# Kernel tuning notes

Measured on AMD Instinct MI355X. Metric: run time of the kernel, lower is better.

The kernel has to match this reference:

```python
import jax, jax.numpy as jnp
import numpy as np

EPS = 1e-12


def setup_inputs() -> dict:
    key = jax.random.key(0)
    k = jax.random.split(key, 6)
    B, C, T, A = 8, 1536, 4096, 128
    x = jax.random.normal(k[0], (B, C, T), dtype=jnp.float32)
    lengths = jax.random.randint(k[1], (B,), T // 2, T + 1, dtype=jnp.int64)
    W1 = jax.random.normal(k[2], (A, 3 * C), dtype=jnp.float32) * (1.0 / np.sqrt(3 * C))
    b1 = jax.random.normal(k[3], (A,), dtype=jnp.float32) * 0.01
    W2 = jax.random.normal(k[4], (1, A), dtype=jnp.float32) * (1.0 / np.sqrt(A))
    b2 = jax.random.normal(k[5], (1,), dtype=jnp.float32) * 0.01
    return {"x": x, "lengths": lengths, "W1": W1, "b1": b1, "W2": W2, "b2": b2}


def reference(x, lengths, W1, b1, W2, b2):
    # x: [B, C, T]
    B, C, T = x.shape
    mask = (jnp.arange(T)[None, :] < lengths[:, None]).astype(x.dtype)  # [B, T]
    m3 = mask[:, None, :]  # [B, 1, T]

    # causal (cumulative) mean / std for global context
    count = jnp.clip(jnp.cumsum(mask, axis=1), 1.0)[:, None, :]        # [B, 1, T]
    causal_mean = jnp.cumsum(x * m3, axis=2) / count                   # [B, C, T]
    causal_var = jnp.cumsum(x * x * m3, axis=2) / count - causal_mean ** 2
    causal_std = jnp.sqrt(jnp.clip(causal_var, EPS))

    attn_in = jnp.concatenate([x, causal_mean, causal_std], axis=1)    # [B, 3C, T]
    attn_in = attn_in.transpose(0, 2, 1)                               # [B, T, 3C]

    h = jnp.tanh(attn_in @ W1.T + b1)                                  # [B, T, A]
    logits = (h @ W2.T + b2)[..., 0]                                   # [B, T]

    # logits are query-independent, so causal softmax row q is
    # exp(l_k) / cumsum(exp(l))_q for k <= q -> O(T*C) prefix scan.
    e = jnp.exp(logits - jnp.max(logits, axis=1, keepdims=True))       # [B, T]
    Z = jnp.cumsum(e, axis=1)[:, None, :]                              # [B, 1, T]
    ew = e[:, None, :]                                                 # [B, 1, T]

    weighted_mean = jnp.cumsum(ew * x, axis=2) / Z                     # [B, C, T]
    sq_diff = (x - weighted_mean) ** 2
    weighted_var = jnp.cumsum(ew * sq_diff, axis=2) / Z
    weighted_std = jnp.sqrt(jnp.clip(weighted_var, EPS))

    # each causal softmax row sums to 1 -> final weights are 1/(T+eps)
    fw = 1.0 / (jnp.asarray(T, x.dtype) + EPS)
    final_mean = jnp.sum(weighted_mean, axis=2) * fw                   # [B, C]
    final_std = jnp.sum(weighted_std, axis=2) * fw
    return jnp.concatenate([final_mean, final_std], axis=1)            # [B, 2C]
```

## Files before the change

kernel.cpp:

```cpp
#include <hip/hip_runtime.h>
#include <hip/hip_bf16.h>

#define B_ 8
#define C_ 1536
#define T_ 4096
#define A_ 128
#define K3_ 4608
#define M32_ 128
#define KP_ 200

typedef _Float16 h8  __attribute__((ext_vector_type(8)));
typedef _Float16 h2v __attribute__((ext_vector_type(2)));
typedef float    f4  __attribute__((ext_vector_type(4)));

__global__ void k0_pack(const float* __restrict__ W1, _Float16* __restrict__ W1f) {
    int i = blockIdx.x * 256 + threadIdx.x;
    if (i >= A_ * K3_) return;
    int a = i / K3_, k = i - a * K3_;
    int t8 = a >> 4, r15 = a & 15;
    int kb = k >> 5, q = (k >> 3) & 3, j = k & 7;
    int lane = q * 16 + r15;
    W1f[(size_t)((kb * 8 + t8) * 64 + lane) * 8 + j] = (_Float16)W1[i];
}

__global__ __launch_bounds__(256) void k1_carry(
    const float* __restrict__ x, const int* __restrict__ lens,
    float2* __restrict__ carry)
{
    const int rowid = blockIdx.x * 4 + (threadIdx.x >> 6);
    const int lane  = threadIdx.x & 63;
    const int b     = rowid / C_;
    const int len   = lens[b];
    const float* xr = x + (size_t)rowid * T_;
    float2* cp = carry + (size_t)rowid * M32_;

    const int grp = lane >> 3;
    float base1 = 0.f, base2 = 0.f;

#pragma unroll
    for (int g = 0; g < 16; ++g) {
        const int t0g = g * 256;
        if (t0g >= len) {
            if ((lane & 7) == 0) cp[g * 8 + grp] = make_float2(base1, base2);
            continue;
        }
        float4 v = *(const float4*)(xr + t0g + lane * 4);
        float s1, s2;
        if (t0g + 256 <= len) {
            s1 = v.x + v.y + v.z + v.w;
            s2 = v.x * v.x + v.y * v.y + v.z * v.z + v.w * v.w;
        } else {
            const int tb = t0g + lane * 4;
            float vs[4] = {v.x, v.y, v.z, v.w};
            s1 = 0.f; s2 = 0.f;
#pragma unroll
            for (int j = 0; j < 4; ++j) {
                float m = (tb + j < len) ? vs[j] : 0.f;
                s1 += m; s2 += m * vs[j];
            }
        }
        float g1 = s1, g2 = s2;
        g1 += __shfl_xor(g1, 1, 64); g2 += __shfl_xor(g2, 1, 64);
        g1 += __shfl_xor(g1, 2, 64); g2 += __shfl_xor(g2, 2, 64);
        g1 += __shfl_xor(g1, 4, 64); g2 += __shfl_xor(g2, 4, 64);
        float V1 = g1, V2 = g2;
#pragma unroll
        for (int d = 8; d < 64; d <<= 1) {
            float o1 = __shfl_up(V1, d, 64);
            float o2 = __shfl_up(V2, d, 64);
            if (lane >= d) { V1 += o1; V2 += o2; }
        }
        const float e1 = V1 - g1, e2 = V2 - g2;
        if ((lane & 7) == 0) {
            cp[g * 8 + grp] = make_float2(base1 + e1, base2 + e2);
        }
        base1 += __shfl(V1, 63, 64);
        base2 += __shfl(V2, 63, 64);
    }
}

__global__ __launch_bounds__(256) void k2_gemm(
    const float* __restrict__ x, const int* __restrict__ lens,
    const float2* __restrict__ carry, const _Float16* __restrict__ W1f,
    const float* __restrict__ b1, const float* __restrict__ W2,
    float* __restrict__ logits)
{
    __shared__ _Float16 tile[32][KP_];
    __shared__ float s_w2[A_], s_b1[A_];
    __shared__ float lpart[2][32];

    const int tid = threadIdx.x;
    const int i    = blockIdx.x;
    const int mlow = i >> 7;
    const int b    = (i >> 4) & 7;
    const int m    = ((i & 15) << 3) | mlow;
    const int t0   = m << 5;
    const int len  = lens[b];

    if (tid < A_) { s_w2[tid] = W2[tid]; s_b1[tid] = b1[tid]; }

    const int cp  = tid >> 3;
    const int sgm = tid & 7;
    const int tb  = t0 + sgm * 4;

    const int lane = tid & 63;
    const int w    = tid >> 6;
    const int mtg  = w & 1;
    const int ntg  = w >> 1;
    const int ln15 = lane & 15, q = lane >> 4;
    const h8* W1f8 = (const h8*)W1f;

    f4 acc[4] = {};

    for (int c0 = 0; c0 < C_; c0 += 64) {
        const size_t rowA = (size_t)b * C_ + c0 + cp * 2;
        const float* xpA = x + rowA * T_ + tb;
        float4 va = *(const float4*)xpA;
        float4 vb = *(const float4*)(xpA + T_);
        float xa[4] = {va.x, va.y, va.z, va.w};
        float xb[4] = {vb.x, vb.y, vb.z, vb.w};
        float pA1[4], pA2[4], pB1[4], pB2[4];
        float a1 = 0.f, a2 = 0.f, c1 = 0.f, c2 = 0.f;
#pragma unroll
        for (int j = 0; j < 4; ++j) {
            bool in = (tb + j) < len;
            float ma = in ? xa[j] : 0.f;
            float mb = in ? xb[j] : 0.f;
            a1 += ma; a2 += ma * xa[j]; pA1[j] = a1; pA2[j] = a2;
            c1 += mb; c2 += mb * xb[j]; pB1[j] = c1; pB2[j] = c2;
        }
        float t1 = a1, t2 = a2, t3 = c1, t4 = c2;
#pragma unroll
        for (int d = 1; d < 8; d <<= 1) {
            float o1 = __shfl_up(t1, d, 8);
            float o2 = __shfl_up(t2, d, 8);
            float o3 = __shfl_up(t3, d, 8);
            float o4 = __shfl_up(t4, d, 8);
            if (sgm >= d) { t1 += o1; t2 += o2; t3 += o3; t4 += o4; }
        }
        const float eA1 = t1 - a1, eA2 = t2 - a2;
        const float eB1 = t3 - c1, eB2 = t4 - c2;
        const float2 crA = carry[rowA * M32_ + m];
        const float2 crB = carry[(rowA + 1) * M32_ + m];
        const int cb = cp >> 2;
        const int co = (cp & 3) * 2;
#pragma unroll
        for (int j = 0; j < 4; ++j) {
            const int t  = tb + j;
            const int tl = sgm * 4 + j;
            float fn = (float)min(t + 1, len);
            float rn = __builtin_amdgcn_rcpf(fn);
            float S1a = crA.x + eA1 + pA1[j];
            float S2a = crA.y + eA2 + pA2[j];
            float mA = S1a * rn;
            float vA = S2a * rn - mA * mA;
            float dA = sqrtf(fmaxf(vA, 1e-12f));
            float S1b = crB.x + eB1 + pB1[j];
            float S2b = crB.y + eB2 + pB2[j];
            float mB = S1b * rn;
            float vB = S2b * rn - mB * mB;
            float dB = sqrtf(fmaxf(vB, 1e-12f));
            const int s  = (tl >> 3) & 3;
            const int xo = ((cb ^ s) << 3) + co;
            h2v px = {(_Float16)xa[j], (_Float16)xb[j]};
            h2v pm = {(_Float16)mA, (_Float16)mB};
            h2v pd = {(_Float16)dA, (_Float16)dB};
            *(h2v*)&tile[tl][xo]       = px;
            *(h2v*)&tile[tl][64 + xo]  = pm;
            *(h2v*)&tile[tl][128 + xo] = pd;
        }
        __syncthreads();
        const int tl = ntg * 16 + ln15;
        const int s  = (tl >> 3) & 3;
        const int kb0 = c0 >> 5;
#pragma unroll
        for (int p = 0; p < 3; ++p) {
#pragma unroll
            for (int kk = 0; kk < 2; ++kk) {
                const int bb = (kk * 4 + q) ^ s;
                h8 bf = *(const h8*)&tile[tl][p * 64 + bb * 8];
                const int kbp = p * 48 + kb0 + kk;
#pragma unroll
                for (int ii = 0; ii < 4; ++ii) {
                    h8 af = W1f8[(kbp * 8 + mtg * 4 + ii) * 64 + lane];
                    acc[ii] = __builtin_amdgcn_mfma_f32_16x16x32_f16(af, bf, acc[ii], 0, 0, 0);
                }
            }
        }
        __syncthreads();
    }
    float pr = 0.f;
#pragma unroll
    for (int ii = 0; ii < 4; ++ii) {
#pragma unroll
        for (int rg = 0; rg < 4; ++rg) {
            int a = (mtg * 4 + ii) * 16 + q * 4 + rg;
            float h = acc[ii][rg] + s_b1[a];
            pr += tanhf(h) * s_w2[a];
        }
    }
    pr += __shfl_xor(pr, 16, 64);
    pr += __shfl_xor(pr, 32, 64);
    if (q == 0) lpart[mtg][ntg * 16 + ln15] = pr;
    __syncthreads();
    if (tid < 32) {
        logits[(size_t)b * T_ + t0 + tid] = lpart[0][tid] + lpart[1][tid];
    }
}

__global__ __launch_bounds__(64) void k3_softmax(
    const float* __restrict__ logits, float* __restrict__ earr,
    float* __restrict__ zarr)
{
    const int b = blockIdx.x;
    const int l = threadIdx.x;
    const float* base = logits + (size_t)b * T_ + l * 64;
    float lg[64];
#pragma unroll
    for (int ii = 0; ii < 16; ++ii) {
        float4 v = *(const float4*)(base + ii * 4);
        lg[ii * 4 + 0] = v.x; lg[ii * 4 + 1] = v.y;
        lg[ii * 4 + 2] = v.z; lg[ii * 4 + 3] = v.w;
    }
    float mx = -3.4e38f;
#pragma unroll
    for (int i = 0; i < 64; ++i) mx = fmaxf(mx, lg[i]);
#pragma unroll
    for (int d = 1; d < 64; d <<= 1) mx = fmaxf(mx, __shfl_xor(mx, d, 64));
    float tot = 0.f;
#pragma unroll
    for (int i = 0; i < 64; ++i) { lg[i] = expf(lg[i] - mx); tot += lg[i]; }
    float V = tot;
#pragma unroll
    for (int d = 1; d < 64; d <<= 1) {
        float o = __shfl_up(V, d, 64);
        if (l >= d) V += o;
    }
    float run = V - tot;
    float* eo = earr + (size_t)b * T_ + l * 64;
    float* zo = zarr + (size_t)b * T_ + l * 64;
#pragma unroll
    for (int ii = 0; ii < 16; ++ii) {
        float4 ev, zv;
        float e0 = lg[ii * 4 + 0]; run += e0; ev.x = e0; zv.x = run;
        float e1 = lg[ii * 4 + 1]; run += e1; ev.y = e1; zv.y = run;
        float e2 = lg[ii * 4 + 2]; run += e2; ev.z = e2; zv.z = run;
        float e3 = lg[ii * 4 + 3]; run += e3; ev.w = e3; zv.w = run;
        *(float4*)(eo + ii * 4) = ev;
        *(float4*)(zo + ii * 4) = zv;
    }
}

__global__ __launch_bounds__(256) void k4_wstats(
    const float* __restrict__ x, const float* __restrict__ earr,
    const float* __restrict__ zarr, float* __restrict__ out)
{
    const int rowid = blockIdx.x * 4 + (threadIdx.x >> 6);
    const int lane  = threadIdx.x & 63;
    const int b = rowid / C_;
    const int c = rowid - b * C_;
    const float* xr = x + (size_t)rowid * T_;
    const float* er = earr + (size_t)b * T_;
    const float* zr = zarr + (size_t)b * T_;

    float am = 0.f, asd = 0.f;
    float baseS = 0.f, baseD = 0.f;

#pragma unroll
    for (int g = 0; g < 16; ++g) {
        const int off = g * 256 + lane * 4;
        float4 xv = *(const float4*)(xr + off);
        float4 ev = *(const float4*)(er + off);
        float4 zv = *(const float4*)(zr + off);
        float s0 = ev.x * xv.x;
        float s1 = s0 + ev.y * xv.y;
        float s2 = s1 + ev.z * xv.z;
        float s3 = s2 + ev.w * xv.w;
        float V = s3;
#pragma unroll
        for (int d = 1; d < 64; d <<= 1) {
            float o = __shfl_up(V, d, 64);
            if (lane >= d) V += o;
        }
        const float Sx = baseS + (V - s3);
        baseS += __shfl(V, 63, 64);
        const float rz0 = __builtin_amdgcn_rcpf(zv.x);
        const float rz1 = __builtin_amdgcn_rcpf(zv.y);
        const float rz2 = __builtin_amdgcn_rcpf(zv.z);
        const float rz3 = __builtin_amdgcn_rcpf(zv.w);
        const float wm0 = (Sx + s0) * rz0;
        const float wm1 = (Sx + s1) * rz1;
        const float wm2 = (Sx + s2) * rz2;
        const float wm3 = (Sx + s3) * rz3;
        am += (wm0 + wm1) + (wm2 + wm3);
        const float d0 = xv.x - wm0;
        const float d1 = xv.y - wm1;
        const float d2 = xv.z - wm2;
        const float d3 = xv.w - wm3;
        float q0 = ev.x * d0 * d0;
        float q1 = q0 + ev.y * d1 * d1;
        float q2 = q1 + ev.z * d2 * d2;
        float q3 = q2 + ev.w * d3 * d3;
        float W = q3;
#pragma unroll
        for (int d = 1; d < 64; d <<= 1) {
            float o = __shfl_up(W, d, 64);
            if (lane >= d) W += o;
        }
        const float Dx = baseD + (W - q3);
        baseD += __shfl(W, 63, 64);
        const float v0 = (Dx + q0) * rz0;
        const float v1 = (Dx + q1) * rz1;
        const float v2 = (Dx + q2) * rz2;
        const float v3 = (Dx + q3) * rz3;
        asd += (sqrtf(fmaxf(v0, 1e-12f)) + sqrtf(fmaxf(v1, 1e-12f)))
             + (sqrtf(fmaxf(v2, 1e-12f)) + sqrtf(fmaxf(v3, 1e-12f)));
    }
#pragma unroll
    for (int d = 1; d < 64; d <<= 1) {
        am  += __shfl_xor(am, d, 64);
        asd += __shfl_xor(asd, d, 64);
    }
    if (lane == 0) {
        out[(size_t)b * (2 * C_) + c]      = am  * (1.f / 4096.f);
        out[(size_t)b * (2 * C_) + C_ + c] = asd * (1.f / 4096.f);
    }
}

extern "C" void kernel_launch(void* const* d_in, const int* in_sizes, int n_in,
                              void* d_out, int out_size, void* d_ws, size_t ws_size,
                              hipStream_t stream) {
    const float* x    = (const float*)d_in[0];
    const int*   lens = (const int*)d_in[1];
    const float* W1   = (const float*)d_in[2];
    const float* b1   = (const float*)d_in[3];
    const float* W2   = (const float*)d_in[4];
    float* out = (float*)d_out;

    char* ws = (char*)d_ws;
    float2*    carry  = (float2*)ws;
    _Float16*  W1f    = (_Float16*)(ws + 12582912);
    float*     logits = (float*)(ws + 13762560);
    float*     earr   = (float*)(ws + 13893632);
    float*     zarr   = (float*)(ws + 14024704);

    k0_pack   <<<(A_ * K3_ + 255) / 256, 256, 0, stream>>>(W1, W1f);
    k1_carry  <<<(B_ * C_) / 4, 256, 0, stream>>>(x, lens, carry);
    k2_gemm   <<<B_ * M32_, 256, 0, stream>>>(x, lens, carry, W1f, b1, W2, logits);
    k3_softmax<<<B_, 64, 0, stream>>>(logits, earr, zarr);
    k4_wstats <<<(B_ * C_) / 4, 256, 0, stream>>>(x, earr, zarr, out);
}
```

Measured before the change: 446.3 us.

## Materialize packed fp16 GEMM operand in a stats kernel; run a pure MFMA GEMM

Adds a new path, used only when the workspace is large enough. A stats kernel computes the causal mean and std per channel and writes x, mean and std as fp16, already swizzled into the MFMA B-fragment layout. A separate pure GEMM kernel then streams that operand and W1 with no in-loop stats work or LDS staging. The softmax kernel is also rewritten to use 1024 threads with a block-wide scan, and it drops the max subtraction before exp. This trades a roughly 300 MB intermediate write and read for a simpler, denser GEMM inner loop, and it risks overflow if logits become large.

```diff
diff --git a/kernel.cpp b/kernel.cpp
--- a/kernel.cpp
+++ b/kernel.cpp
@@ -8,6 +8,8 @@
 #define K3_ 4608
 #define M32_ 128
 #define KP_ 200
+#define NKB_ 144
+#define N16_ 256
 
 typedef _Float16 h8  __attribute__((ext_vector_type(8)));
 typedef _Float16 h2v __attribute__((ext_vector_type(2)));
@@ -23,6 +25,140 @@
     W1f[(size_t)((kb * 8 + t8) * 64 + lane) * 8 + j] = (_Float16)W1[i];
 }
 
+__global__ __launch_bounds__(512) void k1_stats(
+    const float* __restrict__ x, const int* __restrict__ lens,
+    _Float16* __restrict__ P)
+{
+    __shared__ _Float16 lds[768 * 8];
+    const int blk = blockIdx.x;
+    const int b   = blk / 192;
+    const int c8  = blk - b * 192;
+    const int c0  = c8 * 8;
+    const int tid = threadIdx.x, lane = tid & 63, w = tid >> 6;
+    const int len = lens[b];
+    const float* xr = x + ((size_t)b * C_ + c0 + w) * T_;
+    _Float16* Pb = P + (size_t)b * N16_ * NKB_ * 64 * 8;
+    const int q = (c0 >> 3) & 3;
+    const int kb_base = c0 >> 5;
+    const int r16 = tid & 15, grp = tid >> 4;
+
+    float base1 = 0.f, base2 = 0.f;
+    for (int g = 0; g < 16; ++g) {
+        const int t0g = g * 256;
+        const int tb  = t0g + lane * 4;
+        float4 v = *(const float4*)(xr + tb);
+        float vs[4] = {v.x, v.y, v.z, v.w};
+        float p1[4], p2[4];
+        float s1 = 0.f, s2 = 0.f;
+#pragma unroll
+        for (int j = 0; j < 4; ++j) {
+            float xv = vs[j];
+            float mm = (tb + j < len) ? xv : 0.f;
+            s1 += mm; s2 += mm * xv;
+            p1[j] = s1; p2[j] = s2;
+        }
+        float V1 = s1, V2 = s2;
+#pragma unroll
+        for (int d = 1; d < 64; d <<= 1) {
+            float o1 = __shfl_up(V1, d, 64);
+            float o2 = __shfl_up(V2, d, 64);
+            if (lane >= d) { V1 += o1; V2 += o2; }
+        }
+        const float e1 = base1 + (V1 - s1);
+        const float e2 = base2 + (V2 - s2);
+        base1 += __shfl(V1, 63, 64);
+        base2 += __shfl(V2, 63, 64);
+#pragma unroll
+        for (int j = 0; j < 4; ++j) {
+            const int t  = tb + j;
+            const int tl = lane * 4 + j;
+            float S1 = e1 + p1[j], S2 = e2 + p2[j];
+            float rn = __builtin_amdgcn_rcpf((float)min(t + 1, len));
+            float mn = S1 * rn;
+            float var = S2 * rn - mn * mn;
+            float sd = sqrtf(fmaxf(var, 1e-12f));
+            int u0 = tl * 3;
+            int a0 = (u0 + 0) ^ (((u0 + 0) >> 3) & 7);
+            int a1 = (u0 + 1) ^ (((u0 + 1) >> 3) & 7);
+            int a2 = (u0 + 2) ^ (((u0 + 2) >> 3) & 7);
+            lds[a0 * 8 + w] = (_Float16)vs[j];
+            lds[a1 * 8 + w] = (_Float16)mn;
+            lds[a2 * 8 + w] = (_Float16)sd;
+        }
+        __syncthreads();
+#pragma unroll
+        for (int it = 0; it < 2; ++it) {
+            int idx = it * 32 + grp;
+            if (idx < 48) {
+                int n16l = idx / 3, p = idx - n16l * 3;
+                int tl = n16l * 16 + r16;
+                int u = tl * 3 + p;
+                int a = u ^ ((u >> 3) & 7);
+                h8 pay = *(const h8*)&lds[a * 8];
+                int n16 = g * 16 + n16l;
+                int kbp = p * 48 + kb_base;
+                *(h8*)(Pb + (((size_t)(n16 * NKB_ + kbp)) * 64 + q * 16 + r16) * 8) = pay;
+            }
+        }
+        __syncthreads();
+    }
+}
+
+__global__ __launch_bounds__(256) void k2_pure(
+    const _Float16* __restrict__ P, const _Float16* __restrict__ W1f,
+    const float* __restrict__ b1, const float* __restrict__ W2,
+    float* __restrict__ logits)
+{
+    __shared__ float s_w2[A_], s_b1[A_];
+    __shared__ float lpart[2][64];
+    const int tid = threadIdx.x, lane = tid & 63, w = tid >> 6;
+    const int mtg = w & 1, ntg = w >> 1;
+    if (tid < A_) { s_w2[tid] = W2[tid]; s_b1[tid] = b1[tid]; }
+    const int bid = blockIdx.x;
+    const int b   = bid >> 6, t64 = bid & 63;
+    const int n16_0 = t64 * 4 + ntg * 2;
+    const h8* W1f8 = (const h8*)W1f;
+    const h8* p0 = (const h8*)P + (size_t)b * N16_ * NKB_ * 64
+                 + (size_t)(n16_0 + 0) * NKB_ * 64 + lane;
+    const h8* p1 = p0 + (size_t)NKB_ * 64;
+    const h8* wf = W1f8 + mtg * 4 * 64 + lane;
+
+    f4 acc[2][4] = {};
+#pragma unroll 3
+    for (int kb = 0; kb < NKB_; ++kb) {
+        h8 bf0 = p0[kb * 64];
+        h8 bf1 = p1[kb * 64];
+#pragma unroll
+        for (int ii = 0; ii < 4; ++ii) {
+            h8 af = wf[(kb * 8 + ii) * 64];
+            acc[0][ii] = __builtin_amdgcn_mfma_f32_16x16x32_f16(af, bf0, acc[0][ii], 0, 0, 0);
+            acc[1][ii] = __builtin_amdgcn_mfma_f32_16x16x32_f16(af, bf1, acc[1][ii], 0, 0, 0);
+        }
+    }
+    __syncthreads();
+    const int q = lane >> 4, ln15 = lane & 15;
+    float pr[2] = {0.f, 0.f};
+#pragma unroll
+    for (int nn = 0; nn < 2; ++nn) {
+#pragma unroll
+        for (int ii = 0; ii < 4; ++ii) {
+#pragma unroll
+            for (int rg = 0; rg < 4; ++rg) {
+                int a = (mtg * 4 + ii) * 16 + q * 4 + rg;
+                float h = acc[nn][ii][rg] + s_b1[a];
+                pr[nn] += tanhf(h) * s_w2[a];
+            }
+        }
+        pr[nn] += __shfl_xor(pr[nn], 16, 64);
+        pr[nn] += __shfl_xor(pr[nn], 32, 64);
+        if (q == 0) lpart[mtg][ntg * 32 + nn * 16 + ln15] = pr[nn];
+    }
+    __syncthreads();
+    if (tid < 64) {
+        logits[(size_t)b * T_ + t64 * 64 + tid] = lpart[0][tid] + lpart[1][tid];
+    }
+}
+
 __global__ __launch_bounds__(256) void k1_carry(
     const float* __restrict__ x, const int* __restrict__ lens,
     float2* __restrict__ carry)
@@ -33,10 +169,8 @@
     const int len   = lens[b];
     const float* xr = x + (size_t)rowid * T_;
     float2* cp = carry + (size_t)rowid * M32_;
-
     const int grp = lane >> 3;
     float base1 = 0.f, base2 = 0.f;
-
 #pragma unroll
     for (int g = 0; g < 16; ++g) {
         const int t0g = g * 256;
@@ -71,9 +205,7 @@
             if (lane >= d) { V1 += o1; V2 += o2; }
         }
         const float e1 = V1 - g1, e2 = V2 - g2;
-        if ((lane & 7) == 0) {
-            cp[g * 8 + grp] = make_float2(base1 + e1, base2 + e2);
-        }
+        if ((lane & 7) == 0) cp[g * 8 + grp] = make_float2(base1 + e1, base2 + e2);
         base1 += __shfl(V1, 63, 64);
         base2 += __shfl(V2, 63, 64);
     }
@@ -88,7 +220,6 @@
     __shared__ _Float16 tile[32][KP_];
     __shared__ float s_w2[A_], s_b1[A_];
     __shared__ float lpart[2][32];
-
     const int tid = threadIdx.x;
     const int i    = blockIdx.x;
     const int mlow = i >> 7;
@@ -96,22 +227,17 @@
     const int m    = ((i & 15) << 3) | mlow;
     const int t0   = m << 5;
     const int len  = lens[b];
-
     if (tid < A_) { s_w2[tid] = W2[tid]; s_b1[tid] = b1[tid]; }
-
     const int cp  = tid >> 3;
     const int sgm = tid & 7;
     const int tb  = t0 + sgm * 4;
-
     const int lane = tid & 63;
     const int w    = tid >> 6;
     const int mtg  = w & 1;
     const int ntg  = w >> 1;
     const int ln15 = lane & 15, q = lane >> 4;
     const h8* W1f8 = (const h8*)W1f;
-
     f4 acc[4] = {};
-
     for (int c0 = 0; c0 < C_; c0 += 64) {
         const size_t rowA = (size_t)b * C_ + c0 + cp * 2;
         const float* xpA = x + rowA * T_ + tb;
@@ -203,52 +329,37 @@
     pr += __shfl_xor(pr, 32, 64);
     if (q == 0) lpart[mtg][ntg * 16 + ln15] = pr;
     __syncthreads();
-    if (tid < 32) {
-        logits[(size_t)b * T_ + t0 + tid] = lpart[0][tid] + lpart[1][tid];
-    }
-}
-
-__global__ __launch_bounds__(64) void k3_softmax(
+    if (tid < 32) logits[(size_t)b * T_ + t0 + tid] = lpart[0][tid] + lpart[1][tid];
+}
+
+__global__ __launch_bounds__(1024) void k3_softmax(
     const float* __restrict__ logits, float* __restrict__ earr,
     float* __restrict__ zarr)
 {
-    const int b = blockIdx.x;
-    const int l = threadIdx.x;
-    const float* base = logits + (size_t)b * T_ + l * 64;
-    float lg[64];
-#pragma unroll
-    for (int ii = 0; ii < 16; ++ii) {
-        float4 v = *(const float4*)(base + ii * 4);
-        lg[ii * 4 + 0] = v.x; lg[ii * 4 + 1] = v.y;
-        lg[ii * 4 + 2] = v.z; lg[ii * 4 + 3] = v.w;
-    }
-    float mx = -3.4e38f;
-#pragma unroll
-    for (int i = 0; i < 64; ++i) mx = fmaxf(mx, lg[i]);
-#pragma unroll
-    for (int d = 1; d < 64; d <<= 1) mx = fmaxf(mx, __shfl_xor(mx, d, 64));
-    float tot = 0.f;
-#pragma unroll
-    for (int i = 0; i < 64; ++i) { lg[i] = expf(lg[i] - mx); tot += lg[i]; }
-    float V = tot;
+    __shared__ float wsum[16];
+    const int b = blockIdx.x, tid = threadIdx.x, lane = tid & 63, w = tid >> 6;
+    float4 v = *(const float4*)(logits + (size_t)b * T_ + tid * 4);
+    float e0 = expf(v.x), e1 = expf(v.y), e2 = expf(v.z), e3 = expf(v.w);
+    float s = (e0 + e1) + (e2 + e3);
+    float V = s;
 #pragma unroll
     for (int d = 1; d < 64; d <<= 1) {
         float o = __shfl_up(V, d, 64);
-        if (l >= d) V += o;
-    }
-    float run = V - tot;
-    float* eo = earr + (size_t)b * T_ + l * 64;
-    float* zo = zarr + (size_t)b * T_ + l * 64;
-#pragma unroll
-    for (int ii = 0; ii < 16; ++ii) {
-        float4 ev, zv;
-        float e0 = lg[ii * 4 + 0]; run += e0; ev.x = e0; zv.x = run;
-        float e1 = lg[ii * 4 + 1]; run += e1; ev.y = e1; zv.y = run;
-        float e2 = lg[ii * 4 + 2]; run += e2; ev.z = e2; zv.z = run;
-        float e3 = lg[ii * 4 + 3]; run += e3; ev.w = e3; zv.w = run;
-        *(float4*)(eo + ii * 4) = ev;
-        *(float4*)(zo + ii * 4) = zv;
-    }
+        if (lane >= d) V += o;
+    }
+    if (lane == 63) wsum[w] = V;
+    __syncthreads();
+    float wb = 0.f;
+#pragma unroll
+    for (int i = 0; i < 16; ++i) wb += (i < w) ? wsum[i] : 0.f;
+    float run = wb + (V - s);
+    float4 ev, zv;
+    ev.x = e0; run += e0; zv.x = run;
+    ev.y = e1; run += e1; zv.y = run;
+    ev.z = e2; run += e2; zv.z = run;
+    ev.w = e3; run += e3; zv.w = run;
+    *(float4*)(earr + (size_t)b * T_ + tid * 4) = ev;
+    *(float4*)(zarr + (size_t)b * T_ + tid * 4) = zv;
 }
 
 __global__ __launch_bounds__(256) void k4_wstats(
@@ -262,10 +373,8 @@
     const float* xr = x + (size_t)rowid * T_;
     const float* er = earr + (size_t)b * T_;
     const float* zr = zarr + (size_t)b * T_;
-
     float am = 0.f, asd = 0.f;
     float baseS = 0.f, baseD = 0.f;
-
 #pragma unroll
     for (int g = 0; g < 16; ++g) {
         const int off = g * 256 + lane * 4;
@@ -336,17 +445,34 @@
     const float* b1   = (const float*)d_in[3];
     const float* W2   = (const float*)d_in[4];
     float* out = (float*)d_out;
-
     char* ws = (char*)d_ws;
-    float2*    carry  = (float2*)ws;
-    _Float16*  W1f    = (_Float16*)(ws + 12582912);
-    float*     logits = (float*)(ws + 13762560);
-    float*     earr   = (float*)(ws + 13893632);
-    float*     zarr   = (float*)(ws + 14024704);
-
-    k0_pack   <<<(A_ * K3_ + 255) / 256, 256, 0, stream>>>(W1, W1f);
-    k1_carry  <<<(B_ * C_) / 4, 256, 0, stream>>>(x, lens, carry);
-    k2_gemm   <<<B_ * M32_, 256, 0, stream>>>(x, lens, carry, W1f, b1, W2, logits);
-    k3_softmax<<<B_, 64, 0, stream>>>(logits, earr, zarr);
-    k4_wstats <<<(B_ * C_) / 4, 256, 0, stream>>>(x, earr, zarr, out);
-}
+
+    const size_t P_BYTES   = (size_t)B_ * N16_ * NKB_ * 64 * 8 * 2;
+    const size_t W1F_BYTES = (size_t)A_ * K3_ * 2;
+    const size_t LG_BYTES  = (size_t)B_ * T_ * 4;
+    const size_t NEED      = P_BYTES + W1F_BYTES + 3 * LG_BYTES;
+
+    if (ws_size >= NEED) {
+        _Float16* P      = (_Float16*)ws;
+        _Float16* W1f    = (_Float16*)(ws + P_BYTES);
+        float*    logits = (float*)(ws + P_BYTES + W1F_BYTES);
+        float*    earr   = (float*)(ws + P_BYTES + W1F_BYTES + LG_BYTES);
+        float*    zarr   = (float*)(ws + P_BYTES + W1F_BYTES + 2 * LG_BYTES);
+        k0_pack   <<<(A_ * K3_ + 255) / 256, 256, 0, stream>>>(W1, W1f);
+        k1_stats  <<<B_ * (C_ / 8), 512, 0, stream>>>(x, lens, P);
+        k2_pure   <<<B_ * 64, 256, 0, stream>>>(P, W1f, b1, W2, logits);
+        k3_softmax<<<B_, 1024, 0, stream>>>(logits, earr, zarr);
+        k4_wstats <<<(B_ * C_) / 4, 256, 0, stream>>>(x, earr, zarr, out);
+    } else {
+        float2*    carry  = (float2*)ws;
+        _Float16*  W1f    = (_Float16*)(ws + 12582912);
+        float*     logits = (float*)(ws + 13762560);
+        float*     earr   = (float*)(ws + 13893632);
+        float*     zarr   = (float*)(ws + 14024704);
+        k0_pack   <<<(A_ * K3_ + 255) / 256, 256, 0, stream>>>(W1, W1f);
+        k1_carry  <<<(B_ * C_) / 4, 256, 0, stream>>>(x, lens, carry);
+        k2_gemm   <<<B_ * M32_, 256, 0, stream>>>(x, lens, carry, W1f, b1, W2, logits);
+        k3_softmax<<<B_, 1024, 0, stream>>>(logits, earr, zarr);
+        k4_wstats <<<(B_ * C_) / 4, 256, 0, stream>>>(x, earr, zarr, out);
+    }
+}
```

After: 553.2 us. +23.9%, slower.

## Restructure logits GEMM with split-K waves, transposed carries, parallel softmax

Applied to the files above, without the earlier changes.

Replaces the fused stats+GEMM kernel with one where each wave owns 32 time steps and half of the channels. Each W1 fragment is reused across two MFMA N-tiles, each lane does a serial 16-element prefix within its own row, and the two channel halves are combined through shared memory before the tanh/W2 epilogue. A new kernel transposes the carry array so per-time-chunk carries are read contiguously along channels. The softmax scan now uses 1024 threads per batch and drops the max subtraction, which trades global-synchronisation-free parallelism for a reliance on logits staying small enough not to overflow exp.

```diff
diff --git a/kernel.cpp b/kernel.cpp
--- a/kernel.cpp
+++ b/kernel.cpp
@@ -7,10 +7,9 @@
 #define A_ 128
 #define K3_ 4608
 #define M32_ 128
-#define KP_ 200
+#define SCW_ 104
 
 typedef _Float16 h8  __attribute__((ext_vector_type(8)));
-typedef _Float16 h2v __attribute__((ext_vector_type(2)));
 typedef float    f4  __attribute__((ext_vector_type(4)));
 
 __global__ void k0_pack(const float* __restrict__ W1, _Float16* __restrict__ W1f) {
@@ -33,10 +32,8 @@
     const int len   = lens[b];
     const float* xr = x + (size_t)rowid * T_;
     float2* cp = carry + (size_t)rowid * M32_;
-
     const int grp = lane >> 3;
     float base1 = 0.f, base2 = 0.f;
-
 #pragma unroll
     for (int g = 0; g < 16; ++g) {
         const int t0g = g * 256;
@@ -71,184 +68,192 @@
             if (lane >= d) { V1 += o1; V2 += o2; }
         }
         const float e1 = V1 - g1, e2 = V2 - g2;
-        if ((lane & 7) == 0) {
-            cp[g * 8 + grp] = make_float2(base1 + e1, base2 + e2);
-        }
+        if ((lane & 7) == 0) cp[g * 8 + grp] = make_float2(base1 + e1, base2 + e2);
         base1 += __shfl(V1, 63, 64);
         base2 += __shfl(V2, 63, 64);
     }
 }
 
-__global__ __launch_bounds__(256) void k2_gemm(
+__global__ __launch_bounds__(256) void k1b_T(
+    const float2* __restrict__ carry, float2* __restrict__ carryT)
+{
+    __shared__ float2 t[64][65];
+    const int bid = blockIdx.x;
+    const int b = bid / 48;
+    const int r = bid - b * 48;
+    const int ct = r >> 1, mt = r & 1;
+    const int c0 = ct * 64, m0 = mt * 64;
+    const int tx = threadIdx.x & 63, ty = threadIdx.x >> 6;
+#pragma unroll
+    for (int i = 0; i < 16; ++i) {
+        int cl = i * 4 + ty;
+        t[cl][tx] = carry[((size_t)(b * C_ + c0 + cl)) * M32_ + m0 + tx];
+    }
+    __syncthreads();
+#pragma unroll
+    for (int i = 0; i < 16; ++i) {
+        int ml = i * 4 + ty;
+        carryT[((size_t)b * M32_ + m0 + ml) * C_ + c0 + tx] = t[tx][ml];
+    }
+}
+
+__global__ __launch_bounds__(256, 2) void k2f(
     const float* __restrict__ x, const int* __restrict__ lens,
-    const float2* __restrict__ carry, const _Float16* __restrict__ W1f,
+    const float2* __restrict__ carryT, const _Float16* __restrict__ W1f,
     const float* __restrict__ b1, const float* __restrict__ W2,
     float* __restrict__ logits)
 {
-    __shared__ _Float16 tile[32][KP_];
-    __shared__ float s_w2[A_], s_b1[A_];
-    __shared__ float lpart[2][32];
-
-    const int tid = threadIdx.x;
-    const int i    = blockIdx.x;
-    const int mlow = i >> 7;
-    const int b    = (i >> 4) & 7;
-    const int m    = ((i & 15) << 3) | mlow;
-    const int t0   = m << 5;
-    const int len  = lens[b];
-
-    if (tid < A_) { s_w2[tid] = W2[tid]; s_b1[tid] = b1[tid]; }
-
-    const int cp  = tid >> 3;
-    const int sgm = tid & 7;
-    const int tb  = t0 + sgm * 4;
-
-    const int lane = tid & 63;
-    const int w    = tid >> 6;
-    const int mtg  = w & 1;
-    const int ntg  = w >> 1;
-    const int ln15 = lane & 15, q = lane >> 4;
+    __shared__ __align__(16) char smem[32768];
+    __shared__ float s_b1[A_], s_w2[A_];
+
+    const int tid = threadIdx.x, lane = tid & 63, w = tid >> 6;
+    const int s   = w & 1;
+    const int tch = w >> 1;
+    const int bid = blockIdx.x;
+    const int b   = bid >> 6;
+    const int m   = ((bid & 63) << 1) + tch;
+    const int t0  = m << 5;
+    const int len = lens[b];
+    if (tid < A_) { s_b1[tid] = b1[tid]; s_w2[tid] = W2[tid]; }
+
+    const int kc = lane >> 1;
+    const int th = lane & 1;
+    const int c_base = s * 768;
+    _Float16* sc = (_Float16*)smem + w * (32 * SCW_);
     const h8* W1f8 = (const h8*)W1f;
-
-    f4 acc[4] = {};
-
-    for (int c0 = 0; c0 < C_; c0 += 64) {
-        const size_t rowA = (size_t)b * C_ + c0 + cp * 2;
-        const float* xpA = x + rowA * T_ + tb;
-        float4 va = *(const float4*)xpA;
-        float4 vb = *(const float4*)(xpA + T_);
-        float xa[4] = {va.x, va.y, va.z, va.w};
-        float xb[4] = {vb.x, vb.y, vb.z, vb.w};
-        float pA1[4], pA2[4], pB1[4], pB2[4];
-        float a1 = 0.f, a2 = 0.f, c1 = 0.f, c2 = 0.f;
-#pragma unroll
-        for (int j = 0; j < 4; ++j) {
-            bool in = (tb + j) < len;
-            float ma = in ? xa[j] : 0.f;
-            float mb = in ? xb[j] : 0.f;
-            a1 += ma; a2 += ma * xa[j]; pA1[j] = a1; pA2[j] = a2;
-            c1 += mb; c2 += mb * xb[j]; pB1[j] = c1; pB2[j] = c2;
-        }
-        float t1 = a1, t2 = a2, t3 = c1, t4 = c2;
-#pragma unroll
-        for (int d = 1; d < 8; d <<= 1) {
-            float o1 = __shfl_up(t1, d, 8);
-            float o2 = __shfl_up(t2, d, 8);
-            float o3 = __shfl_up(t3, d, 8);
-            float o4 = __shfl_up(t4, d, 8);
-            if (sgm >= d) { t1 += o1; t2 += o2; t3 += o3; t4 += o4; }
-        }
-        const float eA1 = t1 - a1, eA2 = t2 - a2;
-        const float eB1 = t3 - c1, eB2 = t4 - c2;
-        const float2 crA = carry[rowA * M32_ + m];
-        const float2 crB = carry[(rowA + 1) * M32_ + m];
-        const int cb = cp >> 2;
-        const int co = (cp & 3) * 2;
-#pragma unroll
-        for (int j = 0; j < 4; ++j) {
-            const int t  = tb + j;
-            const int tl = sgm * 4 + j;
-            float fn = (float)min(t + 1, len);
-            float rn = __builtin_amdgcn_rcpf(fn);
-            float S1a = crA.x + eA1 + pA1[j];
-            float S2a = crA.y + eA2 + pA2[j];
-            float mA = S1a * rn;
-            float vA = S2a * rn - mA * mA;
-            float dA = sqrtf(fmaxf(vA, 1e-12f));
-            float S1b = crB.x + eB1 + pB1[j];
-            float S2b = crB.y + eB2 + pB2[j];
-            float mB = S1b * rn;
-            float vB = S2b * rn - mB * mB;
-            float dB = sqrtf(fmaxf(vB, 1e-12f));
-            const int s  = (tl >> 3) & 3;
-            const int xo = ((cb ^ s) << 3) + co;
-            h2v px = {(_Float16)xa[j], (_Float16)xb[j]};
-            h2v pm = {(_Float16)mA, (_Float16)mB};
-            h2v pd = {(_Float16)dA, (_Float16)dB};
-            *(h2v*)&tile[tl][xo]       = px;
-            *(h2v*)&tile[tl][64 + xo]  = pm;
-            *(h2v*)&tile[tl][128 + xo] = pd;
-        }
-        __syncthreads();
-        const int tl = ntg * 16 + ln15;
-        const int s  = (tl >> 3) & 3;
-        const int kb0 = c0 >> 5;
+    const bool full = (t0 + 32) <= len;
+    const int tb = t0 + th * 16;
+
+    f4 acc[2][8] = {};
+
+    const float* xptr = x + ((size_t)b * C_ + c_base + kc) * T_ + tb;
+    float4 xv0 = ((const float4*)xptr)[0];
+    float4 xv1 = ((const float4*)xptr)[1];
+    float4 xv2 = ((const float4*)xptr)[2];
+    float4 xv3 = ((const float4*)xptr)[3];
+
+    for (int step = 0; step < 24; ++step) {
+        float xs[16];
+        *(float4*)&xs[0]  = xv0; *(float4*)&xs[4]  = xv1;
+        *(float4*)&xs[8]  = xv2; *(float4*)&xs[12] = xv3;
+        if (step < 23) {
+            xptr += 32 * (size_t)T_;
+            xv0 = ((const float4*)xptr)[0];
+            xv1 = ((const float4*)xptr)[1];
+            xv2 = ((const float4*)xptr)[2];
+            xv3 = ((const float4*)xptr)[3];
+        }
+        const float2 cr =
+            carryT[((size_t)b * M32_ + m) * C_ + c_base + step * 32 + kc];
+
+        float ls1 = 0.f, ls2 = 0.f;
+        if (full) {
+#pragma unroll
+            for (int j = 0; j < 16; ++j) { ls1 += xs[j]; ls2 += xs[j] * xs[j]; }
+        } else {
+#pragma unroll
+            for (int j = 0; j < 16; ++j) {
+                float mv = (tb + j < len) ? xs[j] : 0.f;
+                ls1 += mv; ls2 += mv * xs[j];
+            }
+        }
+        const float o1 = __shfl_xor(ls1, 1, 64);
+        const float o2 = __shfl_xor(ls2, 1, 64);
+        float r1 = cr.x + (th ? o1 : 0.f);
+        float r2 = cr.y + (th ? o2 : 0.f);
+#pragma unroll
+        for (int j = 0; j < 16; ++j) {
+            const float xval = xs[j];
+            const float mv = (full || (tb + j < len)) ? xval : 0.f;
+            r1 += mv; r2 += mv * xval;
+            const float rn = __builtin_amdgcn_rcpf((float)min(tb + j + 1, len));
+            const float mn = r1 * rn;
+            const float var = r2 * rn - mn * mn;
+            const float sd = sqrtf(fmaxf(var, 1e-12f));
+            const int row = th * 16 + j;
+            sc[row * SCW_ + kc]      = (_Float16)xval;
+            sc[row * SCW_ + 32 + kc] = (_Float16)mn;
+            sc[row * SCW_ + 64 + kc] = (_Float16)sd;
+        }
+        const int t15 = lane & 15, k8 = lane >> 4;
+        const int kbS = s * 24 + step;
 #pragma unroll
         for (int p = 0; p < 3; ++p) {
-#pragma unroll
-            for (int kk = 0; kk < 2; ++kk) {
-                const int bb = (kk * 4 + q) ^ s;
-                h8 bf = *(const h8*)&tile[tl][p * 64 + bb * 8];
-                const int kbp = p * 48 + kb0 + kk;
-#pragma unroll
-                for (int ii = 0; ii < 4; ++ii) {
-                    h8 af = W1f8[(kbp * 8 + mtg * 4 + ii) * 64 + lane];
-                    acc[ii] = __builtin_amdgcn_mfma_f32_16x16x32_f16(af, bf, acc[ii], 0, 0, 0);
+            h8 bf0 = *(const h8*)&sc[t15 * SCW_ + p * 32 + k8 * 8];
+            h8 bf1 = *(const h8*)&sc[(16 + t15) * SCW_ + p * 32 + k8 * 8];
+            const int kb = p * 48 + kbS;
+#pragma unroll
+            for (int ii = 0; ii < 8; ++ii) {
+                h8 af = W1f8[(size_t)(kb * 8 + ii) * 64 + lane];
+                acc[0][ii] = __builtin_amdgcn_mfma_f32_16x16x32_f16(af, bf0, acc[0][ii], 0, 0, 0);
+                acc[1][ii] = __builtin_amdgcn_mfma_f32_16x16x32_f16(af, bf1, acc[1][ii], 0, 0, 0);
+            }
+        }
+    }
+
+    __syncthreads();
+    float* red_f = (float*)smem;
+    if (s == 1) {
+        float* r = red_f + tch * 4096;
+#pragma unroll
+        for (int nn = 0; nn < 2; ++nn)
+#pragma unroll
+            for (int ii = 0; ii < 8; ++ii)
+#pragma unroll
+                for (int rg = 0; rg < 4; ++rg)
+                    r[(nn * 32 + ii * 4 + rg) * 64 + lane] = acc[nn][ii][rg];
+    }
+    __syncthreads();
+    if (s == 0) {
+        float* r = red_f + tch * 4096;
+        const int q = lane >> 4;
+#pragma unroll
+        for (int nn = 0; nn < 2; ++nn) {
+            float pr = 0.f;
+#pragma unroll
+            for (int ii = 0; ii < 8; ++ii)
+#pragma unroll
+                for (int rg = 0; rg < 4; ++rg) {
+                    float v = acc[nn][ii][rg] + r[(nn * 32 + ii * 4 + rg) * 64 + lane];
+                    int a = ii * 16 + q * 4 + rg;
+                    pr += tanhf(v + s_b1[a]) * s_w2[a];
                 }
-            }
-        }
-        __syncthreads();
-    }
-    float pr = 0.f;
-#pragma unroll
-    for (int ii = 0; ii < 4; ++ii) {
-#pragma unroll
-        for (int rg = 0; rg < 4; ++rg) {
-            int a = (mtg * 4 + ii) * 16 + q * 4 + rg;
-            float h = acc[ii][rg] + s_b1[a];
-            pr += tanhf(h) * s_w2[a];
-        }
-    }
-    pr += __shfl_xor(pr, 16, 64);
-    pr += __shfl_xor(pr, 32, 64);
-    if (q == 0) lpart[mtg][ntg * 16 + ln15] = pr;
-    __syncthreads();
-    if (tid < 32) {
-        logits[(size_t)b * T_ + t0 + tid] = lpart[0][tid] + lpart[1][tid];
-    }
-}
-
-__global__ __launch_bounds__(64) void k3_softmax(
+            pr += __shfl_xor(pr, 16, 64);
+            pr += __shfl_xor(pr, 32, 64);
+            if (lane < 16)
+                logits[(size_t)b * T_ + t0 + nn * 16 + lane] = pr;
+        }
+    }
+}
+
+__global__ __launch_bounds__(1024) void k3_softmax(
     const float* __restrict__ logits, float* __restrict__ earr,
     float* __restrict__ zarr)
 {
-    const int b = blockIdx.x;
-    const int l = threadIdx.x;
-    const float* base = logits + (size_t)b * T_ + l * 64;
-    float lg[64];
-#pragma unroll
-    for (int ii = 0; ii < 16; ++ii) {
-        float4 v = *(const float4*)(base + ii * 4);
-        lg[ii * 4 + 0] = v.x; lg[ii * 4 + 1] = v.y;
-        lg[ii * 4 + 2] = v.z; lg[ii * 4 + 3] = v.w;
-    }
-    float mx = -3.4e38f;
-#pragma unroll
-    for (int i = 0; i < 64; ++i) mx = fmaxf(mx, lg[i]);
-#pragma unroll
-    for (int d = 1; d < 64; d <<= 1) mx = fmaxf(mx, __shfl_xor(mx, d, 64));
-    float tot = 0.f;
-#pragma unroll
-    for (int i = 0; i < 64; ++i) { lg[i] = expf(lg[i] - mx); tot += lg[i]; }
-    float V = tot;
+    __shared__ float wsum[16];
+    const int b = blockIdx.x, tid = threadIdx.x, lane = tid & 63, w = tid >> 6;
+    float4 v = *(const float4*)(logits + (size_t)b * T_ + tid * 4);
+    float e0 = expf(v.x), e1 = expf(v.y), e2 = expf(v.z), e3 = expf(v.w);
+    float s = (e0 + e1) + (e2 + e3);
+    float V = s;
 #pragma unroll
     for (int d = 1; d < 64; d <<= 1) {
         float o = __shfl_up(V, d, 64);
-        if (l >= d) V += o;
-    }
-    float run = V - tot;
-    float* eo = earr + (size_t)b * T_ + l * 64;
-    float* zo = zarr + (size_t)b * T_ + l * 64;
-#pragma unroll
-    for (int ii = 0; ii < 16; ++ii) {
-        float4 ev, zv;
-        float e0 = lg[ii * 4 + 0]; run += e0; ev.x = e0; zv.x = run;
-        float e1 = lg[ii * 4 + 1]; run += e1; ev.y = e1; zv.y = run;
-        float e2 = lg[ii * 4 + 2]; run += e2; ev.z = e2; zv.z = run;
-        float e3 = lg[ii * 4 + 3]; run += e3; ev.w = e3; zv.w = run;
-        *(float4*)(eo + ii * 4) = ev;
-        *(float4*)(zo + ii * 4) = zv;
-    }
+        if (lane >= d) V += o;
+    }
+    if (lane == 63) wsum[w] = V;
+    __syncthreads();
+    float wb = 0.f;
+#pragma unroll
+    for (int i = 0; i < 16; ++i) wb += (i < w) ? wsum[i] : 0.f;
+    float run = wb + (V - s);
+    float4 ev, zv;
+    ev.x = e0; run += e0; zv.x = run;
+    ev.y = e1; run += e1; zv.y = run;
+    ev.z = e2; run += e2; zv.z = run;
+    ev.w = e3; run += e3; zv.w = run;
+    *(float4*)(earr + (size_t)b * T_ + tid * 4) = ev;
+    *(float4*)(zarr + (size_t)b * T_ + tid * 4) = zv;
 }
 
 __global__ __launch_bounds__(256) void k4_wstats(
@@ -262,10 +267,8 @@
     const float* xr = x + (size_t)rowid * T_;
     const float* er = earr + (size_t)b * T_;
     const float* zr = zarr + (size_t)b * T_;
-
     float am = 0.f, asd = 0.f;
     float baseS = 0.f, baseD = 0.f;
-
 #pragma unroll
     for (int g = 0; g < 16; ++g) {
         const int off = g * 256 + lane * 4;
@@ -336,17 +339,19 @@
     const float* b1   = (const float*)d_in[3];
     const float* W2   = (const float*)d_in[4];
     float* out = (float*)d_out;
-
     char* ws = (char*)d_ws;
+
     float2*    carry  = (float2*)ws;
-    _Float16*  W1f    = (_Float16*)(ws + 12582912);
-    float*     logits = (float*)(ws + 13762560);
-    float*     earr   = (float*)(ws + 13893632);
-    float*     zarr   = (float*)(ws + 14024704);
+    float2*    carryT = (float2*)(ws + 12582912);
+    _Float16*  W1f    = (_Float16*)(ws + 25165824);
+    float*     logits = (float*)(ws + 26345472);
+    float*     earr   = (float*)(ws + 26476544);
+    float*     zarr   = (float*)(ws + 26607616);
 
     k0_pack   <<<(A_ * K3_ + 255) / 256, 256, 0, stream>>>(W1, W1f);
     k1_carry  <<<(B_ * C_) / 4, 256, 0, stream>>>(x, lens, carry);
-    k2_gemm   <<<B_ * M32_, 256, 0, stream>>>(x, lens, carry, W1f, b1, W2, logits);
-    k3_softmax<<<B_, 64, 0, stream>>>(logits, earr, zarr);
+    k1b_T     <<<B_ * 48, 256, 0, stream>>>(carry, carryT);
+    k2f       <<<B_ * 64, 256, 0, stream>>>(x, lens, carryT, W1f, b1, W2, logits);
+    k3_softmax<<<B_, 1024, 0, stream>>>(logits, earr, zarr);
     k4_wstats <<<(B_ * C_) / 4, 256, 0, stream>>>(x, earr, zarr, out);
 }
```

Result: slower. 470.9 us (+5.5%).
